# Optimization experiments

Hardware: AMD Instinct MI355X
Metric: run time of the kernel (lower is better)

The kernel has to match this reference:

```python
import jax, jax.numpy as jnp
import numpy as np

# DeformConv (RegSeg): offset conv + mask conv (sigmoid) + modulated deformable conv v2
STRIDE = 1
PAD = 1
DIL = 1
G = 1          # deformable_groups
KH, KW = 3, 3


def _conv(x, w, b):
    # standard NCHW conv, stride/pad/dilation of the module
    y = jax.lax.conv_general_dilated(
        x, w, window_strides=(STRIDE, STRIDE),
        padding=((PAD, PAD), (PAD, PAD)), rhs_dilation=(DIL, DIL),
        dimension_numbers=("NCHW", "OIHW", "NCHW"))
    return y + b[None, :, None, None]


def _deform_conv2d(x, offset, mask, w, b):
    # torchvision DeformConv2d (modulated, v2) semantics
    B, C, H, W = x.shape
    O = w.shape[0]
    K = KH * KW
    Ho = (H + 2 * PAD - DIL * (KH - 1) - 1) // STRIDE + 1
    Wo = (W + 2 * PAD - DIL * (KW - 1) - 1) // STRIDE + 1
    Cg = C // G

    # base sampling grid: p0 + p_k
    ky = jnp.repeat(jnp.arange(KH), KW) * DIL            # [K]
    kx = jnp.tile(jnp.arange(KW), KH) * DIL              # [K]
    oy = jnp.arange(Ho) * STRIDE - PAD                   # [Ho]
    ox = jnp.arange(Wo) * STRIDE - PAD                   # [Wo]
    base_y = (ky[:, None, None] + oy[None, :, None]).astype(x.dtype)  # [K,Ho,1]
    base_x = (kx[:, None, None] + ox[None, None, :]).astype(x.dtype)  # [K,1,Wo]

    off = offset.reshape(B, G, K, 2, Ho, Wo)             # channel layout: g, k, (dy,dx)
    py = base_y[None, None] + off[:, :, :, 0]            # [B,G,K,Ho,Wo]
    px = base_x[None, None] + off[:, :, :, 1]
    m = mask.reshape(B, G, K, Ho, Wo)

    imgf = x.reshape(B * G, Cg, H * W)
    y0 = jnp.floor(py).astype(jnp.int32)
    x0 = jnp.floor(px).astype(jnp.int32)
    ly = py - y0.astype(x.dtype)
    lx = px - x0.astype(x.dtype)

    def corner(iy, ix, wgt):
        # zero-padded bilinear corner: out-of-bounds corners contribute 0
        valid = (iy >= 0) & (iy < H) & (ix >= 0) & (ix < W)
        idx = (jnp.clip(iy, 0, H - 1) * W + jnp.clip(ix, 0, W - 1)).reshape(B * G, -1)
        g = jax.vmap(lambda im, ii: im[:, ii])(imgf, idx)            # [B*G,Cg,K*Ho*Wo]
        g = g.reshape(B, G, Cg, K, Ho, Wo)
        return g * (wgt * valid.astype(x.dtype))[:, :, None]          # [B,G,Cg,K,Ho,Wo]

    val = (corner(y0,     x0,     (1 - ly) * (1 - lx))
         + corner(y0,     x0 + 1, (1 - ly) * lx)
         + corner(y0 + 1, x0,     ly * (1 - lx))
         + corner(y0 + 1, x0 + 1, ly * lx))
    val = val * m[:, :, None]                                         # modulation

    wr = w.reshape(O, G, Cg, K)
    out = jnp.einsum("bgckpq,ogck->bopq", val, wr) + b[None, :, None, None]
    return out


def setup_inputs() -> dict:
    key = jax.random.key(0)
    ks = jax.random.split(key, 8)
    B, C, H, W, O = 4, 128, 96, 96, 128
    K = KH * KW
    fan = 1.0 / np.sqrt(C * K)
    return {
        "x":        jax.random.normal(ks[0], (B, C, H, W), jnp.float32),
        "x2":       jax.random.normal(ks[1], (B, C, H, W), jnp.float32),
        "offset_w": jax.random.normal(ks[2], (2 * G * K, C, KH, KW), jnp.float32) * 0.01,
        "offset_b": jax.random.normal(ks[3], (2 * G * K,), jnp.float32) * 0.01,
        "mask_w":   jax.random.normal(ks[4], (G * K, C, KH, KW), jnp.float32) * 0.05,
        "mask_b":   jnp.zeros((G * K,), jnp.float32),
        "deform_w": jax.random.normal(ks[5], (O, C, KH, KW), jnp.float32) * fan,
        "deform_b": jax.random.normal(ks[6], (O,), jnp.float32) * fan,
    }


def reference(x, x2, offset_w, offset_b, mask_w, mask_b, deform_w, deform_b):
    offset = _conv(x2, offset_w, offset_b)
    mask = jax.nn.sigmoid(_conv(x2, mask_w, mask_b))
    return _deform_conv2d(x, offset, mask, deform_w, deform_b)
```

## Files before the change

kernel.cpp:

```cpp
#include <hip/hip_runtime.h>

#define CIN   128
#define HH    96
#define WW    96
#define OUTC  128
#define HWSZ  9216
#define KK    9
#define KTOT  1152

typedef _Float16 f16x8 __attribute__((ext_vector_type(8)));
typedef _Float16 h2    __attribute__((ext_vector_type(2)));
typedef float    f32x4 __attribute__((ext_vector_type(4)));

__device__ __forceinline__ unsigned short f2h(float f) {
  _Float16 h = (_Float16)f;
  return __builtin_bit_cast(unsigned short, h);
}
__device__ __forceinline__ unsigned pack_h(float v0, float v1) {
  auto r = __builtin_amdgcn_cvt_pkrtz(v0, v1);
  return __builtin_bit_cast(unsigned, r);
}

#define WT2B_O 147456
#define BIAS_O 184320
#define XN_O   184384
#define X2N_O  (184384 + 4718592)

__global__ __launch_bounds__(256) void prep_all(
    const float* __restrict__ x, const float* __restrict__ x2,
    const float* __restrict__ offw, const float* __restrict__ maskw,
    const float* __restrict__ defw, const float* __restrict__ offb,
    const float* __restrict__ maskb, void* __restrict__ wsv) {
  int bid = blockIdx.x;
  int t = threadIdx.x;
  if (bid < 1152) {
    __shared__ unsigned short tile[64][136];
    int tsel = bid / 576;
    int rem = bid - tsel * 576;
    int b = rem / 144;
    int hw0 = (rem % 144) * 64;
    const float* src = tsel ? x2 : x;
    unsigned short* dst = (unsigned short*)wsv + (tsel ? X2N_O : XN_O);
    unsigned* tw = (unsigned*)&tile[0][0];
    int c2  = t & 15;
    int px4 = t >> 4;
#pragma unroll
    for (int pass = 0; pass < 4; ++pass) {
      int c = pass * 32 + c2 * 2;
      const float* r0 = src + ((size_t)(b * CIN + c)) * HWSZ + hw0 + px4 * 4;
      float4 f0 = *(const float4*)r0;
      float4 f1 = *(const float4*)(r0 + HWSZ);
      int wb = pass * 16 + c2;
      tw[(px4 * 4 + 0) * 68 + wb] = pack_h(f0.x, f1.x);
      tw[(px4 * 4 + 1) * 68 + wb] = pack_h(f0.y, f1.y);
      tw[(px4 * 4 + 2) * 68 + wb] = pack_h(f0.z, f1.z);
      tw[(px4 * 4 + 3) * 68 + wb] = pack_h(f0.w, f1.w);
    }
    __syncthreads();
    unsigned* drow = (unsigned*)(dst + ((size_t)(b * HWSZ + hw0)) * 128);
    int w4 = t & 15, pxr = t >> 4;
#pragma unroll
    for (int pass = 0; pass < 4; ++pass) {
      int px = pass * 16 + pxr;
      uint4 v = *(const uint4*)&tw[px * 68 + w4 * 4];
      *(uint4*)&drow[(size_t)px * 64 + w4 * 4] = v;
    }
    return;
  }
  unsigned short* wtb  = (unsigned short*)wsv;
  unsigned short* wt2b = wtb + WT2B_O;
  float* bias32 = (float*)(wtb + BIAS_O);
  int idx = (bid - 1152) * 256 + t;
  if (idx < OUTC * KTOT) {
    int o = idx / KTOT, r = idx - o * KTOT;
    int c = r / KK, tap = r - c * KK;
    wtb[o * KTOT + tap * 128 + c] = f2h(defw[idx]);
  } else if (idx < OUTC * KTOT + 32 * KTOT) {
    int j = idx - OUTC * KTOT;
    int oc = j / KTOT, r = j - oc * KTOT;
    int c = r / KK, tap = r - c * KK;
    float v = 0.f;
    if (oc < 18)      v = offw[j];
    else if (oc < 27) v = maskw[j - 18 * KTOT];
    wt2b[oc * KTOT + tap * 128 + c] = f2h(v);
  } else if (idx < OUTC * KTOT + 32 * KTOT + 32) {
    int j = idx - OUTC * KTOT - 32 * KTOT;
    float v = 0.f;
    if (j < 18) v = offb[j]; else if (j < 27) v = maskb[j - 18];
    bias32[j] = v;
  }
}

__global__ __launch_bounds__(256, 3) void fused(
    const float* __restrict__ defb, const void* __restrict__ wsv,
    float* __restrict__ out) {
  const unsigned short* wtb  = (const unsigned short*)wsv;
  const unsigned short* wt2b = wtb + WT2B_O;
  const float* bias32 = (const float*)(wtb + BIAS_O);
  const unsigned short* xn  = wtb + XN_O;
  const unsigned short* x2n = wtb + X2N_O;

  __shared__ unsigned bw[64 * 68];
  __shared__ unsigned short val[64][136];
  __shared__ float om[32][68];
  __shared__ unsigned sidxw[KK * 4 * 64];

  int t = threadIdx.x;
  int w = t >> 6;
  int l15 = t & 15, quad = (t >> 4) & 3;
  int rb = blockIdx.x;
  int bid = (rb & 7) * 72 + (rb >> 3);
  int b = bid / 144;
  int pblk = (bid % 144) * 64;

  int phg[4], pwg[4];
#pragma unroll
  for (int G = 0; G < 4; ++G) {
    int p = pblk + w * 16 + G * 4 + quad;
    phg[G] = p / WW;
    pwg[G] = p - phg[G] * WW;
  }

  f32x4 oa0 = {0.f, 0.f, 0.f, 0.f};
  f32x4 oa1 = {0.f, 0.f, 0.f, 0.f};
  const unsigned short* x2nb = x2n + ((size_t)b * HWSZ) * 128;
  for (int tap = 0; tap < KK; ++tap) {
    int ky = tap / 3 - 1, kx = tap % 3 - 1;
    uint4 vG[4];
#pragma unroll
    for (int G = 0; G < 4; ++G) {
      int y = phg[G] + ky, xx = pwg[G] + kx;
      bool ok = ((unsigned)y < HH) && ((unsigned)xx < WW);
      int pos = ok ? (y * WW + xx) : 0;
      uint4 v = *(const uint4*)(x2nb + ((size_t)pos << 7) + l15 * 8);
      vG[G] = ok ? v : make_uint4(0u, 0u, 0u, 0u);
    }
#pragma unroll
    for (int j = 0; j < 2; ++j) {
      int cc = t + 256 * j;
      int row = cc >> 4, c16 = cc & 15;
      *(uint4*)&bw[row * 68 + c16 * 4] =
          *(const uint4*)(wt2b + (size_t)row * KTOT + tap * 128 + c16 * 8);
    }
#pragma unroll
    for (int G = 0; G < 4; ++G)
      *(uint4*)&val[w * 16 + G * 4 + quad][l15 * 8] = vG[G];
    __syncthreads();
#pragma unroll
    for (int ks = 0; ks < 4; ++ks) {
      f16x8 af = *(const f16x8*)&val[w * 16 + l15][ks * 32 + quad * 8];
      f16x8 b0 = *(const f16x8*)&bw[(size_t)l15 * 68 + ks * 16 + quad * 4];
      f16x8 b1 = *(const f16x8*)&bw[(size_t)(l15 + 16) * 68 + ks * 16 + quad * 4];
      oa0 = __builtin_amdgcn_mfma_f32_16x16x32_f16(af, b0, oa0, 0, 0, 0);
      oa1 = __builtin_amdgcn_mfma_f32_16x16x32_f16(af, b1, oa1, 0, 0, 0);
    }
    __syncthreads();
  }
#pragma unroll
  for (int nt = 0; nt < 2; ++nt) {
    f32x4 a = nt ? oa1 : oa0;
    int oc = nt * 16 + l15;
    float bia = bias32[oc];
#pragma unroll
    for (int r = 0; r < 4; ++r)
      om[oc][w * 16 + quad * 4 + r] = a[r] + bia;
  }
  __syncthreads();

  for (int e = t; e < KK * 64; e += 256) {
    int tap = e >> 6, pp = e & 63;
    int gp2 = pblk + pp;
    int h = gp2 / WW, ww_ = gp2 % WW;
    float dy = om[2 * tap][pp], dx = om[2 * tap + 1][pp];
    float mr = om[18 + tap][pp];
    float m = 1.f / (1.f + __expf(-mr));
    float py  = (float)(h + tap / 3 - 1) + dy;
    float pxx = (float)(ww_ + tap % 3 - 1) + dx;
    float y0f = floorf(py), x0f = floorf(pxx);
    int y0 = (int)y0f, x0 = (int)x0f;
    float ly = py - y0f, lx = pxx - x0f;
    int y1 = y0 + 1, x1 = x0 + 1;
    bool vy0 = (unsigned)y0 < HH, vy1 = (unsigned)y1 < HH;
    bool vx0 = (unsigned)x0 < WW, vx1 = (unsigned)x1 < WW;
    int cy0 = min(max(y0, 0), HH - 1), cy1 = min(max(y1, 0), HH - 1);
    int cx0 = min(max(x0, 0), WW - 1), cx1 = min(max(x1, 0), WW - 1);
    unsigned i00 = cy0 * WW + cx0, i01 = cy0 * WW + cx1;
    unsigned i10 = cy1 * WW + cx0, i11 = cy1 * WW + cx1;
    float w00 = (vy0 && vx0) ? m * (1.f - ly) * (1.f - lx) : 0.f;
    float w01 = (vy0 && vx1) ? m * (1.f - ly) * lx         : 0.f;
    float w10 = (vy1 && vx0) ? m * ly * (1.f - lx)         : 0.f;
    float w11 = (vy1 && vx1) ? m * ly * lx                 : 0.f;
    sidxw[(tap * 4 + 0) * 64 + pp] = i00 | ((unsigned)f2h(w00) << 16);
    sidxw[(tap * 4 + 1) * 64 + pp] = i01 | ((unsigned)f2h(w01) << 16);
    sidxw[(tap * 4 + 2) * 64 + pp] = i10 | ((unsigned)f2h(w10) << 16);
    sidxw[(tap * 4 + 3) * 64 + pp] = i11 | ((unsigned)f2h(w11) << 16);
  }
  __syncthreads();

  f32x4 acc[8];
#pragma unroll
  for (int nt = 0; nt < 8; ++nt) acc[nt] = (f32x4){0.f, 0.f, 0.f, 0.f};
  const unsigned short* xnb = xn + ((size_t)b * HWSZ) * 128;

  for (int tap = 0; tap < KK; ++tap) {
    unsigned sw[4][4];
#pragma unroll
    for (int cr = 0; cr < 4; ++cr)
#pragma unroll
      for (int G = 0; G < 4; ++G)
        sw[cr][G] = sidxw[(tap * 4 + cr) * 64 + w * 16 + G * 4 + quad];
    uint4 v[4][4];
#pragma unroll
    for (int G = 0; G < 4; ++G)
#pragma unroll
      for (int cr = 0; cr < 4; ++cr)
        v[cr][G] = *(const uint4*)(xnb + ((size_t)(sw[cr][G] & 0xffffu) << 7) + l15 * 8);
#pragma unroll
    for (int G = 0; G < 4; ++G) {
      h2 f[4];
#pragma unroll
      for (int j = 0; j < 4; ++j) f[j] = (h2){(_Float16)0.f, (_Float16)0.f};
#pragma unroll
      for (int cr = 0; cr < 4; ++cr) {
        _Float16 wh =
            __builtin_bit_cast(_Float16, (unsigned short)(sw[cr][G] >> 16));
        h2 wpk = {wh, wh};
        const h2* a = (const h2*)&v[cr][G];
#pragma unroll
        for (int j = 0; j < 4; ++j)
          f[j] += wpk * a[j];
      }
      *(uint4*)&val[w * 16 + G * 4 + quad][l15 * 8] =
          make_uint4(__builtin_bit_cast(unsigned, f[0]),
                     __builtin_bit_cast(unsigned, f[1]),
                     __builtin_bit_cast(unsigned, f[2]),
                     __builtin_bit_cast(unsigned, f[3]));
    }
#pragma unroll
    for (int j = 0; j < 4; ++j) {
      int cc = t + 256 * j;
      int row = cc >> 4, c16 = cc & 15;
      *(uint4*)&bw[row * 68 + c16 * 4] =
          *(const uint4*)(wtb + (size_t)row * KTOT + tap * 128 + c16 * 8);
    }
    __syncthreads();
    f16x8 af[4];
#pragma unroll
    for (int ks = 0; ks < 4; ++ks)
      af[ks] = *(const f16x8*)&val[w * 16 + l15][ks * 32 + quad * 8];
#pragma unroll
    for (int ks = 0; ks < 4; ++ks)
#pragma unroll
      for (int nt = 0; nt < 4; ++nt) {
        f16x8 bb = *(const f16x8*)&bw[(size_t)(nt * 16 + l15) * 68 + ks * 16 + quad * 4];
        acc[nt] = __builtin_amdgcn_mfma_f32_16x16x32_f16(af[ks], bb, acc[nt], 0, 0, 0);
      }
    __syncthreads();
#pragma unroll
    for (int j = 0; j < 4; ++j) {
      int cc = t + 256 * j;
      int row = cc >> 4, c16 = cc & 15;
      *(uint4*)&bw[row * 68 + c16 * 4] =
          *(const uint4*)(wtb + (size_t)(64 + row) * KTOT + tap * 128 + c16 * 8);
    }
    __syncthreads();
#pragma unroll
    for (int ks = 0; ks < 4; ++ks)
#pragma unroll
      for (int nt = 0; nt < 4; ++nt) {
        f16x8 bb = *(const f16x8*)&bw[(size_t)(nt * 16 + l15) * 68 + ks * 16 + quad * 4];
        acc[4 + nt] = __builtin_amdgcn_mfma_f32_16x16x32_f16(af[ks], bb, acc[4 + nt], 0, 0, 0);
      }
    __syncthreads();
  }

  for (int r = 0; r < 4; ++r) {
    f32x4 a0 = acc[2 * r], a1 = acc[2 * r + 1];
    float db0 = defb[r * 32 + l15];
    float db1 = defb[r * 32 + 16 + l15];
    if (r) __syncthreads();
#pragma unroll
    for (int reg = 0; reg < 4; ++reg) {
      om[l15]     [w * 16 + quad * 4 + reg] = a0[reg] + db0;
      om[16 + l15][w * 16 + quad * 4 + reg] = a1[reg] + db1;
    }
    __syncthreads();
    int row = t >> 4;
    int col4 = (t & 15) * 4;
#pragma unroll
    for (int hrow = 0; hrow < 2; ++hrow) {
      int rr = row + hrow * 16;
      float4 vv = *(float4*)&om[rr][col4];
      *(float4*)&out[((size_t)b * OUTC + r * 32 + rr) * HWSZ + pblk + col4] = vv;
    }
  }
}

extern "C" void kernel_launch(void* const* d_in, const int* in_sizes, int n_in,
                              void* d_out, int out_size, void* d_ws, size_t ws_size,
                              hipStream_t stream) {
  const float* x     = (const float*)d_in[0];
  const float* x2    = (const float*)d_in[1];
  const float* offw  = (const float*)d_in[2];
  const float* offb  = (const float*)d_in[3];
  const float* maskw = (const float*)d_in[4];
  const float* maskb = (const float*)d_in[5];
  const float* defw  = (const float*)d_in[6];
  const float* defb  = (const float*)d_in[7];
  float* out = (float*)d_out;

  hipLaunchKernelGGL(prep_all, dim3(1873), dim3(256), 0, stream,
                     x, x2, offw, maskw, defw, offb, maskb, d_ws);
  hipLaunchKernelGGL(fused, dim3(576), dim3(256), 0, stream, defb, d_ws, out);
}
```

Before: 145.7 us.

## Gather MFMA A-operands directly into registers and load full weight tile per tap

Remaps thread-to-pixel assignment so each lane gathers the exact channels it feeds into the MFMA A operand, eliminating the val shared-memory staging buffer and its writes and reads for both the offset/mask conv and the deformable conv. The weight tile for all 128 output channels is now loaded into a doubled LDS buffer at once, removing one pair of barriers per tap. The trade-off is more shared memory per block, which may lower occupancy, and more live registers per thread. Per-lane global loads are also now strided across channel chunks rather than contiguous across lanes, which may hurt coalescing.

After: 178.9 us. +22.8%, slower.

```diff
diff --git a/kernel.cpp b/kernel.cpp
--- a/kernel.cpp
+++ b/kernel.cpp
@@ -100,8 +100,7 @@
   const unsigned short* xn  = wtb + XN_O;
   const unsigned short* x2n = wtb + X2N_O;
 
-  __shared__ unsigned bw[64 * 68];
-  __shared__ unsigned short val[64][136];
+  __shared__ unsigned bw[128 * 68];
   __shared__ float om[32][68];
   __shared__ unsigned sidxw[KK * 4 * 64];
 
@@ -113,28 +112,22 @@
   int b = bid / 144;
   int pblk = (bid % 144) * 64;
 
-  int phg[4], pwg[4];
-#pragma unroll
-  for (int G = 0; G < 4; ++G) {
-    int p = pblk + w * 16 + G * 4 + quad;
-    phg[G] = p / WW;
-    pwg[G] = p - phg[G] * WW;
-  }
+  int prow = pblk + w * 16 + l15;
+  int ph = prow / WW;
+  int pw_ = prow - ph * WW;
 
   f32x4 oa0 = {0.f, 0.f, 0.f, 0.f};
   f32x4 oa1 = {0.f, 0.f, 0.f, 0.f};
   const unsigned short* x2nb = x2n + ((size_t)b * HWSZ) * 128;
   for (int tap = 0; tap < KK; ++tap) {
     int ky = tap / 3 - 1, kx = tap % 3 - 1;
-    uint4 vG[4];
-#pragma unroll
-    for (int G = 0; G < 4; ++G) {
-      int y = phg[G] + ky, xx = pwg[G] + kx;
-      bool ok = ((unsigned)y < HH) && ((unsigned)xx < WW);
-      int pos = ok ? (y * WW + xx) : 0;
-      uint4 v = *(const uint4*)(x2nb + ((size_t)pos << 7) + l15 * 8);
-      vG[G] = ok ? v : make_uint4(0u, 0u, 0u, 0u);
-    }
+    int y = ph + ky, xx = pw_ + kx;
+    bool ok = ((unsigned)y < HH) && ((unsigned)xx < WW);
+    int pos = ok ? (y * WW + xx) : 0;
+    const unsigned short* p = x2nb + ((size_t)pos << 7) + quad * 8;
+    uint4 u[4];
+#pragma unroll
+    for (int ks = 0; ks < 4; ++ks) u[ks] = *(const uint4*)(p + ks * 32);
 #pragma unroll
     for (int j = 0; j < 2; ++j) {
       int cc = t + 256 * j;
@@ -142,13 +135,12 @@
       *(uint4*)&bw[row * 68 + c16 * 4] =
           *(const uint4*)(wt2b + (size_t)row * KTOT + tap * 128 + c16 * 8);
     }
-#pragma unroll
-    for (int G = 0; G < 4; ++G)
-      *(uint4*)&val[w * 16 + G * 4 + quad][l15 * 8] = vG[G];
     __syncthreads();
 #pragma unroll
     for (int ks = 0; ks < 4; ++ks) {
-      f16x8 af = *(const f16x8*)&val[w * 16 + l15][ks * 32 + quad * 8];
+      uint4 m = u[ks];
+      if (!ok) m = make_uint4(0u, 0u, 0u, 0u);
+      f16x8 af = __builtin_bit_cast(f16x8, m);
       f16x8 b0 = *(const f16x8*)&bw[(size_t)l15 * 68 + ks * 16 + quad * 4];
       f16x8 b1 = *(const f16x8*)&bw[(size_t)(l15 + 16) * 68 + ks * 16 + quad * 4];
       oa0 = __builtin_amdgcn_mfma_f32_16x16x32_f16(af, b0, oa0, 0, 0, 0);
@@ -203,73 +195,57 @@
   const unsigned short* xnb = xn + ((size_t)b * HWSZ) * 128;
 
   for (int tap = 0; tap < KK; ++tap) {
-    unsigned sw[4][4];
+    unsigned sw[4];
 #pragma unroll
     for (int cr = 0; cr < 4; ++cr)
-#pragma unroll
-      for (int G = 0; G < 4; ++G)
-        sw[cr][G] = sidxw[(tap * 4 + cr) * 64 + w * 16 + G * 4 + quad];
+      sw[cr] = sidxw[(tap * 4 + cr) * 64 + w * 16 + l15];
     uint4 v[4][4];
 #pragma unroll
-    for (int G = 0; G < 4; ++G)
-#pragma unroll
-      for (int cr = 0; cr < 4; ++cr)
-        v[cr][G] = *(const uint4*)(xnb + ((size_t)(sw[cr][G] & 0xffffu) << 7) + l15 * 8);
-#pragma unroll
-    for (int G = 0; G < 4; ++G) {
-      h2 f[4];
-#pragma unroll
-      for (int j = 0; j < 4; ++j) f[j] = (h2){(_Float16)0.f, (_Float16)0.f};
-#pragma unroll
-      for (int cr = 0; cr < 4; ++cr) {
-        _Float16 wh =
-            __builtin_bit_cast(_Float16, (unsigned short)(sw[cr][G] >> 16));
-        h2 wpk = {wh, wh};
-        const h2* a = (const h2*)&v[cr][G];
-#pragma unroll
-        for (int j = 0; j < 4; ++j)
-          f[j] += wpk * a[j];
-      }
-      *(uint4*)&val[w * 16 + G * 4 + quad][l15 * 8] =
-          make_uint4(__builtin_bit_cast(unsigned, f[0]),
-                     __builtin_bit_cast(unsigned, f[1]),
-                     __builtin_bit_cast(unsigned, f[2]),
-                     __builtin_bit_cast(unsigned, f[3]));
-    }
-#pragma unroll
-    for (int j = 0; j < 4; ++j) {
+    for (int cr = 0; cr < 4; ++cr) {
+      const unsigned short* p =
+          xnb + ((size_t)(sw[cr] & 0xffffu) << 7) + quad * 8;
+#pragma unroll
+      for (int ks = 0; ks < 4; ++ks)
+        v[cr][ks] = *(const uint4*)(p + ks * 32);
+    }
+#pragma unroll
+    for (int j = 0; j < 8; ++j) {
       int cc = t + 256 * j;
       int row = cc >> 4, c16 = cc & 15;
       *(uint4*)&bw[row * 68 + c16 * 4] =
           *(const uint4*)(wtb + (size_t)row * KTOT + tap * 128 + c16 * 8);
     }
-    __syncthreads();
     f16x8 af[4];
 #pragma unroll
+    for (int ks = 0; ks < 4; ++ks) {
+      h2 f[4];
+#pragma unroll
+      for (int j = 0; j < 4; ++j) f[j] = (h2){(_Float16)0.f, (_Float16)0.f};
+#pragma unroll
+      for (int cr = 0; cr < 4; ++cr) {
+        _Float16 wh =
+            __builtin_bit_cast(_Float16, (unsigned short)(sw[cr] >> 16));
+        h2 wpk = {wh, wh};
+        const h2* a = (const h2*)&v[cr][ks];
+#pragma unroll
+        for (int j = 0; j < 4; ++j)
+          f[j] += wpk * a[j];
+      }
+      uint4 u = make_uint4(__builtin_bit_cast(unsigned, f[0]),
+                           __builtin_bit_cast(unsigned, f[1]),
+                           __builtin_bit_cast(unsigned, f[2]),
+                           __builtin_bit_cast(unsigned, f[3]));
+      af[ks] = __builtin_bit_cast(f16x8, u);
+    }
+    __syncthreads();
+#pragma unroll
     for (int ks = 0; ks < 4; ++ks)
-      af[ks] = *(const f16x8*)&val[w * 16 + l15][ks * 32 + quad * 8];
-#pragma unroll
-    for (int ks = 0; ks < 4; ++ks)
-#pragma unroll
-      for (int nt = 0; nt < 4; ++nt) {
-        f16x8 bb = *(const f16x8*)&bw[(size_t)(nt * 16 + l15) * 68 + ks * 16 + quad * 4];
-        acc[nt] = __builtin_amdgcn_mfma_f32_16x16x32_f16(af[ks], bb, acc[nt], 0, 0, 0);
-      }
-    __syncthreads();
-#pragma unroll
-    for (int j = 0; j < 4; ++j) {
-      int cc = t + 256 * j;
-      int row = cc >> 4, c16 = cc & 15;
-      *(uint4*)&bw[row * 68 + c16 * 4] =
-          *(const uint4*)(wtb + (size_t)(64 + row) * KTOT + tap * 128 + c16 * 8);
-    }
-    __syncthreads();
-#pragma unroll
-    for (int ks = 0; ks < 4; ++ks)
-#pragma unroll
-      for (int nt = 0; nt < 4; ++nt) {
-        f16x8 bb = *(const f16x8*)&bw[(size_t)(nt * 16 + l15) * 68 + ks * 16 + quad * 4];
-        acc[4 + nt] = __builtin_amdgcn_mfma_f32_16x16x32_f16(af[ks], bb, acc[4 + nt], 0, 0, 0);
+#pragma unroll
+      for (int nt = 0; nt < 8; ++nt) {
+        f16x8 bb = *(const f16x8*)&bw[(size_t)(nt * 16 + l15) * 68 +
+                                      ks * 16 + quad * 4];
+        acc[nt] =
+            __builtin_amdgcn_mfma_f32_16x16x32_f16(af[ks], bb, acc[nt], 0, 0, 0);
       }
     __syncthreads();
   }
```
